# Performance work log

Measured on AMD Instinct MI355X. Metric: run time of the kernel, lower is better.

Reference implementation:

```python
import jax, jax.numpy as jnp
import numpy as np

N_NODES = 100000
LATENT_DIM = 8
SAMPLE_SIZE = 8192
N_EDGES = 1000000
EPS = 1e-6


def setup_inputs() -> dict:
    key = jax.random.key(0)
    k1, k2, k3, k4, k5 = jax.random.split(key, 5)
    latent_Z = jax.random.normal(k1, (N_NODES, LATENT_DIM), dtype=jnp.float32)
    alpha = jax.random.normal(k2, (1,), dtype=jnp.float32)
    sample_idx = jax.random.randint(k3, (SAMPLE_SIZE,), 0, N_NODES, dtype=jnp.int64)
    sparse_sample_i = jax.random.randint(k4, (N_EDGES,), 0, N_NODES, dtype=jnp.int64)
    sparse_sample_j = jax.random.randint(k5, (N_EDGES,), 0, N_NODES, dtype=jnp.int64)
    return {"latent_Z": latent_Z, "alpha": alpha, "sample_idx": sample_idx,
            "sparse_sample_i": sparse_sample_i, "sparse_sample_j": sparse_sample_j}


def reference(latent_Z, alpha, sample_idx, sparse_sample_i, sparse_sample_j):
    # --- dense non-edge term over the sampled subgraph ---
    Zs = latent_Z[sample_idx]                              # [S, D]
    diff = Zs[:, None, :] - Zs[None, :, :] + EPS           # [S, S, D]
    dist = jnp.sqrt(jnp.sum(diff * diff, axis=-1))         # [S, S]
    mat = jnp.exp(-dist)                                   # [S, S]
    # original uses exp(ones) vectors in the matmul-with-ones trick -> factor e^2
    ones_exp_sq = jnp.exp(jnp.float32(1.0)) ** 2
    offdiag_sum = jnp.sum(mat) - jnp.sum(jnp.diagonal(mat))
    z_pdist1 = jnp.exp(alpha[0]) * 0.5 * ones_exp_sq * offdiag_sum
    # --- sparse positive-edge term ---
    ed = latent_Z[sparse_sample_i] - latent_Z[sparse_sample_j] + EPS  # [E, D]
    edist = jnp.sqrt(jnp.sum(ed * ed, axis=-1))                        # [E]
    z_pdist2 = jnp.sum(-edist + alpha[0])
    return z_pdist2 - z_pdist1
```

## Files before the change

### kernel.cpp

```cpp
#include <hip/hip_runtime.h>
#include <hip/hip_bf16.h>
#include <math.h>

#define NNODES   100000
#define S        8192
#define D        8
#define EPSF     1e-6f
#define LOG2E    1.442695040888963f
#define EPS_S    (LOG2E * EPSF)
#define NT       512

#define ZHL_OFF  0
#define U_OFF    262144
#define V_OFF    294912
#define DP_OFF   327680
#define SP_OFF   334848
#define ZB_OFF   335872

#define NSBLK    256
#define NDBLK    1792
#define NWPP     28

typedef __attribute__((ext_vector_type(8))) short short8_t;
typedef __attribute__((ext_vector_type(4))) float f32x4;

__device__ __forceinline__ float block_reduce_f(float v, float* sm) {
    #pragma unroll
    for (int off = 32; off > 0; off >>= 1) v += __shfl_down(v, off, 64);
    int lane = threadIdx.x & 63, wid = threadIdx.x >> 6;
    if (lane == 0) sm[wid] = v;
    __syncthreads();
    float s = 0.f;
    if (threadIdx.x == 0) {
        for (int w = 0; w < 4; ++w) s += sm[w];
    }
    return s;
}

__global__ __launch_bounds__(256) void gather_kernel(const float* __restrict__ Z,
                                                     const int* __restrict__ idx,
                                                     ushort* __restrict__ zhl,
                                                     float* __restrict__ u,
                                                     float* __restrict__ v,
                                                     ushort* __restrict__ zb16) {
    int gid = blockIdx.x * 256 + threadIdx.x;

    if (gid < S) {
        int n = idx[gid];
        const float4* zp = (const float4*)(Z + (size_t)n * D);
        float4 a = zp[0], b = zp[1];
        float z[8] = { a.x, a.y, a.z, a.w, b.x, b.y, b.z, b.w };
        float ss = 0.f;
        short8_t h, l;
        #pragma unroll
        for (int k = 0; k < 8; ++k) {
            float zs = LOG2E * z[k];
            ss = fmaf(zs, zs, ss);
            __hip_bfloat16 hb = __float2bfloat16(zs);
            float hf = __bfloat162float(hb);
            __hip_bfloat16 lb = __float2bfloat16(zs - hf);
            h[k] = (short)__builtin_bit_cast(unsigned short, hb);
            l[k] = (short)__builtin_bit_cast(unsigned short, lb);
        }
        *(short8_t*)(zhl + (size_t)gid * 16)     = h;
        *(short8_t*)(zhl + (size_t)gid * 16 + 8) = l;
        u[gid] = ss + 8.f * EPS_S * EPS_S;
        v[gid] = ss;
    }

    if (gid < NNODES) {
        const float4* zp = (const float4*)(Z + (size_t)gid * D);
        float4 a = zp[0], b = zp[1];
        float z[8] = { a.x, a.y, a.z, a.w, b.x, b.y, b.z, b.w };
        short8_t o;
        #pragma unroll
        for (int k = 0; k < 8; ++k) {
            __hip_bfloat16 bb = __float2bfloat16(z[k]);
            o[k] = (short)__builtin_bit_cast(unsigned short, bb);
        }
        *(short8_t*)(zb16 + (size_t)gid * 8) = o;
    }
}

#define UNPACK8(u4, f)                                        \
    f[0] = __uint_as_float(u4.x << 16);                       \
    f[1] = __uint_as_float(u4.x & 0xffff0000u);               \
    f[2] = __uint_as_float(u4.y << 16);                       \
    f[3] = __uint_as_float(u4.y & 0xffff0000u);               \
    f[4] = __uint_as_float(u4.z << 16);                       \
    f[5] = __uint_as_float(u4.z & 0xffff0000u);               \
    f[6] = __uint_as_float(u4.w << 16);                       \
    f[7] = __uint_as_float(u4.w & 0xffff0000u);

__device__ __forceinline__ float edge_dist4(const uint4* __restrict__ zb,
                                            int4 ia, int4 ib) {
    float acc = 0.f;
    int aidx[4] = { ia.x, ia.y, ia.z, ia.w };
    int bidx[4] = { ib.x, ib.y, ib.z, ib.w };
    #pragma unroll
    for (int q = 0; q < 4; ++q) {
        uint4 ua = zb[aidx[q]];
        uint4 ub = zb[bidx[q]];
        float fa[8], fb[8];
        UNPACK8(ua, fa);
        UNPACK8(ub, fb);
        float s2 = 0.f;
        #pragma unroll
        for (int k = 0; k < 8; ++k) {
            float d = fa[k] - fb[k] + EPSF;
            s2 = fmaf(d, d, s2);
        }
        acc += __builtin_amdgcn_sqrtf(s2);
    }
    return acc;
}

__device__ __forceinline__ void dense_sweep(const ushort* __restrict__ zhl,
                                            const float* __restrict__ v,
                                            short8_t afrag, float4 u4, int boff,
                                            int ti, int tj0, int cnt, int r,
                                            float& ax, float& ay, float& az, float& aw) {
    const ushort* bp = zhl + (size_t)(tj0 * 16 + r) * 16 + boff;
    const float*  vp = v + tj0 * 16 + r;
    short8_t bnext = *(const short8_t*)bp;
    float    vnext = vp[0];
    #pragma unroll 4
    for (int t = 0; t < cnt; ++t) {
        short8_t bcur = bnext;
        float    vcur = vnext;
        if (t + 1 < cnt) {
            bnext = *(const short8_t*)(bp + (size_t)(t + 1) * 256);
            vnext = vp[(t + 1) * 16];
        }
        float w = (tj0 + t == ti) ? 1.f : 2.f;
        f32x4 c = { 0.f, 0.f, 0.f, 0.f };
        c = __builtin_amdgcn_mfma_f32_16x16x32_bf16(afrag, bcur, c, 0, 0, 0);
        float d2_0 = fmaf(c[0], -2.f, u4.x + vcur);
        float d2_1 = fmaf(c[1], -2.f, u4.y + vcur);
        float d2_2 = fmaf(c[2], -2.f, u4.z + vcur);
        float d2_3 = fmaf(c[3], -2.f, u4.w + vcur);
        ax = fmaf(w, __builtin_amdgcn_exp2f(-__builtin_amdgcn_sqrtf(__builtin_fabsf(d2_0))), ax);
        ay = fmaf(w, __builtin_amdgcn_exp2f(-__builtin_amdgcn_sqrtf(__builtin_fabsf(d2_1))), ay);
        az = fmaf(w, __builtin_amdgcn_exp2f(-__builtin_amdgcn_sqrtf(__builtin_fabsf(d2_2))), az);
        aw = fmaf(w, __builtin_amdgcn_exp2f(-__builtin_amdgcn_sqrtf(__builtin_fabsf(d2_3))), aw);
    }
}

__global__ __launch_bounds__(256) void fused_kernel(
        const ushort* __restrict__ zhl, const float* __restrict__ u,
        const float* __restrict__ v, const ushort* __restrict__ zb16,
        const int* __restrict__ ei, const int* __restrict__ ej, int ne,
        float* __restrict__ dpart, float* __restrict__ spart) {
    __shared__ float red[4];
    int tid = threadIdx.x, bx = blockIdx.x;

    if (bx < NSBLK) {
        const uint4* zb = (const uint4*)zb16;
        float acc = 0.f;
        int nchunk = ne >> 2;
        int stride = NSBLK * 256;
        int c = bx * 256 + tid;
        if (c < nchunk) {
            int4 ia = ((const int4*)ei)[c];
            int4 ib = ((const int4*)ej)[c];
            while (true) {
                int cn = c + stride;
                int4 ian, ibn;
                bool more = cn < nchunk;
                if (more) {
                    ian = ((const int4*)ei)[cn];
                    ibn = ((const int4*)ej)[cn];
                }
                acc += edge_dist4(zb, ia, ib);
                if (!more) break;
                ia = ian; ib = ibn; c = cn;
            }
        }
        for (int e = (nchunk << 2) + bx * 256 + tid; e < ne; e += stride) {
            uint4 ua = zb[ei[e]];
            uint4 ub = zb[ej[e]];
            float fa[8], fb[8];
            UNPACK8(ua, fa);
            UNPACK8(ub, fb);
            float s2 = 0.f;
            #pragma unroll
            for (int k = 0; k < 8; ++k) {
                float d = fa[k] - fb[k] + EPSF;
                s2 = fmaf(d, d, s2);
            }
            acc += __builtin_amdgcn_sqrtf(s2);
        }
        float s = block_reduce_f(acc, red);
        if (tid == 0) spart[bx] = s;
        return;
    }

    int dbx  = bx - NSBLK;
    int wave = tid >> 6, lane = tid & 63;
    int g = lane >> 4, r = lane & 15;
    int p  = dbx / 7;
    int wv = (dbx - p * 7) * 4 + wave;
    int k0 = (wv * 513) / NWPP;
    int k1 = ((wv + 1) * 513) / NWPP;
    int n1 = NT - p;
    int boff = (g >> 1) * 8;

    float ax = 0.f, ay = 0.f, az = 0.f, aw = 0.f;

    int eA = k1 < n1 ? k1 : n1;
    if (k0 < eA) {
        int ti = p;
        short8_t afrag = *(const short8_t*)(zhl + (size_t)(ti * 16 + r) * 16 + (g & 1) * 8);
        float4 u4 = *(const float4*)(u + ti * 16 + g * 4);
        dense_sweep(zhl, v, afrag, u4, boff, ti, p + k0, eA - k0, r, ax, ay, az, aw);
    }
    int sB = k0 > n1 ? k0 : n1;
    if (sB < k1) {
        int ti = (NT - 1) - p;
        short8_t afrag = *(const short8_t*)(zhl + (size_t)(ti * 16 + r) * 16 + (g & 1) * 8);
        float4 u4 = *(const float4*)(u + ti * 16 + g * 4);
        dense_sweep(zhl, v, afrag, u4, boff, ti, ti + (sB - n1), k1 - sB, r, ax, ay, az, aw);
    }
    float s = block_reduce_f((ax + ay) + (az + aw), red);
    if (tid == 0) dpart[dbx] = s;
}

__global__ __launch_bounds__(256) void final_kernel(const float* __restrict__ alpha,
                                                    const float* __restrict__ dpart,
                                                    const float* __restrict__ spart,
                                                    float* __restrict__ out,
                                                    int ne) {
    __shared__ double rd[4], rs[4];
    double ds = 0.0, ss = 0.0;
    for (int k = threadIdx.x; k < NDBLK; k += 256) ds += (double)dpart[k];
    for (int k = threadIdx.x; k < NSBLK; k += 256) ss += (double)spart[k];
    #pragma unroll
    for (int off = 32; off > 0; off >>= 1) {
        ds += __shfl_down(ds, off, 64);
        ss += __shfl_down(ss, off, 64);
    }
    int lane = threadIdx.x & 63, wid = threadIdx.x >> 6;
    if (lane == 0) { rd[wid] = ds; rs[wid] = ss; }
    __syncthreads();
    if (threadIdx.x == 0) {
        double Dsum = 0.0, Ssum = 0.0;
        for (int w = 0; w < 4; ++w) { Dsum += rd[w]; Ssum += rs[w]; }
        double trace = (double)S * exp(-sqrt(8.0) * (double)EPSF);
        double offdiag = Dsum - trace;
        double a = (double)alpha[0];
        double z_pdist2 = (double)ne * a - Ssum;
        double z_pdist1 = exp(a) * 0.5 * 7.3890560989306495 * offdiag;
        out[0] = (float)(z_pdist2 - z_pdist1);
    }
}

extern "C" void kernel_launch(void* const* d_in, const int* in_sizes, int n_in,
                              void* d_out, int out_size, void* d_ws, size_t ws_size,
                              hipStream_t stream) {
    const float* latent_Z = (const float*)d_in[0];
    const float* alpha    = (const float*)d_in[1];
    const int*   sidx     = (const int*)d_in[2];
    const int*   ei       = (const int*)d_in[3];
    const int*   ej       = (const int*)d_in[4];
    int ne = in_sizes[3];
    float* out = (float*)d_out;
    char*  ws  = (char*)d_ws;

    ushort* zhl   = (ushort*)(ws + ZHL_OFF);
    float*  u     = (float*)(ws + U_OFF);
    float*  v     = (float*)(ws + V_OFF);
    float*  dpart = (float*)(ws + DP_OFF);
    float*  spart = (float*)(ws + SP_OFF);
    ushort* zb16  = (ushort*)(ws + ZB_OFF);

    gather_kernel<<<(NNODES + 255) / 256, 256, 0, stream>>>(latent_Z, sidx,
                                                            zhl, u, v, zb16);
    fused_kernel<<<NSBLK + NDBLK, 256, 0, stream>>>(zhl, u, v, zb16, ei, ej, ne,
                                                    dpart, spart);
    final_kernel<<<1, 256, 0, stream>>>(alpha, dpart, spart, out, ne);
}
```

Measured before the change: 33.76 us.

## Switch dense pairwise tile from 16x16 to 32x32 MFMA tiles

Replaces the 16x16x32 bf16 MFMA per tile with two 32x32x16 bf16 MFMAs (hi/lo halves) over 32-row tiles. The tile count drops to 256, the triangular work split and block count are recomputed to match, and each lane now evaluates 16 pairwise distances per step instead of 4. The goal is to amortise B-fragment loads and loop overhead over more outputs. The cost is more accumulator registers and a different load pattern, which may lower occupancy.

After: 30.21 us. -10.5%, faster.

```diff
diff --git a/kernel.cpp b/kernel.cpp
--- a/kernel.cpp
+++ b/kernel.cpp
@@ -8,21 +8,21 @@
 #define EPSF     1e-6f
 #define LOG2E    1.442695040888963f
 #define EPS_S    (LOG2E * EPSF)
-#define NT       512
+#define NT2      256
 
 #define ZHL_OFF  0
 #define U_OFF    262144
 #define V_OFF    294912
 #define DP_OFF   327680
-#define SP_OFF   334848
-#define ZB_OFF   335872
+#define SP_OFF   331776
+#define ZB_OFF   332800
 
 #define NSBLK    256
-#define NDBLK    1792
-#define NWPP     28
-
-typedef __attribute__((ext_vector_type(8))) short short8_t;
-typedef __attribute__((ext_vector_type(4))) float f32x4;
+#define NDBLK    1024
+#define NWPP     32
+
+typedef __attribute__((ext_vector_type(8)))  short short8_t;
+typedef __attribute__((ext_vector_type(16))) float f32x16;
 
 __device__ __forceinline__ float block_reduce_f(float v, float* sm) {
     #pragma unroll
@@ -115,34 +115,43 @@
     return acc;
 }
 
-__device__ __forceinline__ void dense_sweep(const ushort* __restrict__ zhl,
-                                            const float* __restrict__ v,
-                                            short8_t afrag, float4 u4, int boff,
-                                            int ti, int tj0, int cnt, int r,
-                                            float& ax, float& ay, float& az, float& aw) {
-    const ushort* bp = zhl + (size_t)(tj0 * 16 + r) * 16 + boff;
-    const float*  vp = v + tj0 * 16 + r;
-    short8_t bnext = *(const short8_t*)bp;
-    float    vnext = vp[0];
-    #pragma unroll 4
+__device__ __forceinline__ void dense_sweep32(const ushort* __restrict__ zhl,
+                                              const float* __restrict__ v,
+                                              short8_t afrag, const float4* u4,
+                                              int ti, int tj0, int cnt, int c31,
+                                              float& ax, float& ay, float& az, float& aw) {
+    const ushort* bp = zhl + (size_t)(tj0 * 32 + c31) * 16;
+    const float*  vp = v + tj0 * 32 + c31;
+    short8_t bh = *(const short8_t*)bp;
+    short8_t bl = *(const short8_t*)(bp + 8);
+    float    vt = vp[0];
+    #pragma unroll 2
     for (int t = 0; t < cnt; ++t) {
-        short8_t bcur = bnext;
-        float    vcur = vnext;
+        short8_t bhc = bh, blc = bl;
+        float    vtc = vt;
         if (t + 1 < cnt) {
-            bnext = *(const short8_t*)(bp + (size_t)(t + 1) * 256);
-            vnext = vp[(t + 1) * 16];
+            bh = *(const short8_t*)(bp + (size_t)(t + 1) * 512);
+            bl = *(const short8_t*)(bp + (size_t)(t + 1) * 512 + 8);
+            vt = vp[(t + 1) * 32];
         }
         float w = (tj0 + t == ti) ? 1.f : 2.f;
-        f32x4 c = { 0.f, 0.f, 0.f, 0.f };
-        c = __builtin_amdgcn_mfma_f32_16x16x32_bf16(afrag, bcur, c, 0, 0, 0);
-        float d2_0 = fmaf(c[0], -2.f, u4.x + vcur);
-        float d2_1 = fmaf(c[1], -2.f, u4.y + vcur);
-        float d2_2 = fmaf(c[2], -2.f, u4.z + vcur);
-        float d2_3 = fmaf(c[3], -2.f, u4.w + vcur);
-        ax = fmaf(w, __builtin_amdgcn_exp2f(-__builtin_amdgcn_sqrtf(__builtin_fabsf(d2_0))), ax);
-        ay = fmaf(w, __builtin_amdgcn_exp2f(-__builtin_amdgcn_sqrtf(__builtin_fabsf(d2_1))), ay);
-        az = fmaf(w, __builtin_amdgcn_exp2f(-__builtin_amdgcn_sqrtf(__builtin_fabsf(d2_2))), az);
-        aw = fmaf(w, __builtin_amdgcn_exp2f(-__builtin_amdgcn_sqrtf(__builtin_fabsf(d2_3))), aw);
+        f32x16 c = { 0.f, 0.f, 0.f, 0.f, 0.f, 0.f, 0.f, 0.f,
+                     0.f, 0.f, 0.f, 0.f, 0.f, 0.f, 0.f, 0.f };
+        c = __builtin_amdgcn_mfma_f32_32x32x16_bf16(afrag, bhc, c, 0, 0, 0);
+        c = __builtin_amdgcn_mfma_f32_32x32x16_bf16(afrag, blc, c, 0, 0, 0);
+        #pragma unroll
+        for (int q = 0; q < 4; ++q) {
+            float s0 = u4[q].x + vtc, s1 = u4[q].y + vtc;
+            float s2 = u4[q].z + vtc, s3 = u4[q].w + vtc;
+            float d0 = fmaf(c[4*q+0], -2.f, s0);
+            float d1 = fmaf(c[4*q+1], -2.f, s1);
+            float d2 = fmaf(c[4*q+2], -2.f, s2);
+            float d3 = fmaf(c[4*q+3], -2.f, s3);
+            ax = fmaf(w, __builtin_amdgcn_exp2f(-__builtin_amdgcn_sqrtf(__builtin_fabsf(d0))), ax);
+            ay = fmaf(w, __builtin_amdgcn_exp2f(-__builtin_amdgcn_sqrtf(__builtin_fabsf(d1))), ay);
+            az = fmaf(w, __builtin_amdgcn_exp2f(-__builtin_amdgcn_sqrtf(__builtin_fabsf(d2))), az);
+            aw = fmaf(w, __builtin_amdgcn_exp2f(-__builtin_amdgcn_sqrtf(__builtin_fabsf(d3))), aw);
+        }
     }
 }
 
@@ -197,29 +206,33 @@
 
     int dbx  = bx - NSBLK;
     int wave = tid >> 6, lane = tid & 63;
-    int g = lane >> 4, r = lane & 15;
-    int p  = dbx / 7;
-    int wv = (dbx - p * 7) * 4 + wave;
-    int k0 = (wv * 513) / NWPP;
-    int k1 = ((wv + 1) * 513) / NWPP;
-    int n1 = NT - p;
-    int boff = (g >> 1) * 8;
+    int g = lane >> 5, c31 = lane & 31;
+
+    int p  = dbx >> 3;
+    int wv = (dbx & 7) * 4 + wave;
+    int k0 = (wv * 257) / NWPP;
+    int k1 = ((wv + 1) * 257) / NWPP;
+    int n1 = NT2 - p;
 
     float ax = 0.f, ay = 0.f, az = 0.f, aw = 0.f;
 
     int eA = k1 < n1 ? k1 : n1;
     if (k0 < eA) {
         int ti = p;
-        short8_t afrag = *(const short8_t*)(zhl + (size_t)(ti * 16 + r) * 16 + (g & 1) * 8);
-        float4 u4 = *(const float4*)(u + ti * 16 + g * 4);
-        dense_sweep(zhl, v, afrag, u4, boff, ti, p + k0, eA - k0, r, ax, ay, az, aw);
+        short8_t afrag = *(const short8_t*)(zhl + (size_t)(ti * 32 + c31) * 16 + g * 8);
+        float4 u4[4];
+        #pragma unroll
+        for (int q = 0; q < 4; ++q) u4[q] = *(const float4*)(u + ti * 32 + 8 * q + 4 * g);
+        dense_sweep32(zhl, v, afrag, u4, ti, p + k0, eA - k0, c31, ax, ay, az, aw);
     }
     int sB = k0 > n1 ? k0 : n1;
     if (sB < k1) {
-        int ti = (NT - 1) - p;
-        short8_t afrag = *(const short8_t*)(zhl + (size_t)(ti * 16 + r) * 16 + (g & 1) * 8);
-        float4 u4 = *(const float4*)(u + ti * 16 + g * 4);
-        dense_sweep(zhl, v, afrag, u4, boff, ti, ti + (sB - n1), k1 - sB, r, ax, ay, az, aw);
+        int ti = (NT2 - 1) - p;
+        short8_t afrag = *(const short8_t*)(zhl + (size_t)(ti * 32 + c31) * 16 + g * 8);
+        float4 u4[4];
+        #pragma unroll
+        for (int q = 0; q < 4; ++q) u4[q] = *(const float4*)(u + ti * 32 + 8 * q + 4 * g);
+        dense_sweep32(zhl, v, afrag, u4, ti, ti + (sB - n1), k1 - sB, c31, ax, ay, az, aw);
     }
     float s = block_reduce_f((ax + ay) + (az + aw), red);
     if (tid == 0) dpart[dbx] = s;
```
